# Optimization experiments

Hardware: AMD Instinct MI355X
Metric: run time of the kernel (lower is better)

The kernel has to match this reference:

```python
import jax, jax.numpy as jnp
import numpy as np

SIGMA = 5.0
LOSS_WEIGHT = 1.0


def setup_inputs() -> dict:
    key = jax.random.key(0)
    k1, k2, k3, k4 = jax.random.split(key, 4)
    bs, nj, h, w, d = 4, 22, 64, 64, 64
    return {
        "kpts_gt": jax.random.normal(k1, (bs, 3, nj), dtype=jnp.float32),
        "kpts_pred": jax.random.normal(k2, (bs, 3, nj), dtype=jnp.float32),
        "heatmaps": jax.random.normal(k3, (bs, nj, h, w, d), dtype=jnp.float32),
        "grids": jax.random.normal(k4, (bs, h * w * d, 3), dtype=jnp.float32),
    }


def reference(kpts_gt, kpts_pred, heatmaps, grids):
    bs, nj, h, w, d = heatmaps.shape
    # grids: [bs, h*w*d, 3] -> [bs, 3, h, w, d]
    g = grids.transpose(0, 2, 1).reshape(bs, 3, h, w, d)
    # squared distance via expansion |g - c|^2 = |g|^2 - 2 g.c + |c|^2
    # avoids materializing a [bs, nj, 3, h, w, d] diff tensor
    g2 = jnp.sum(g * g, axis=1)                      # [bs, h, w, d]
    c2 = jnp.sum(kpts_pred * kpts_pred, axis=1)      # [bs, nj]
    gc = jnp.einsum("bchwd,bcj->bjhwd", g, kpts_pred)  # [bs, nj, h, w, d]
    d2 = g2[:, None] - 2.0 * gc + c2[:, :, None, None, None]
    # NOTE: faithful to the original code, the /(2*sigma^2) is applied to the
    # exp result, NOT inside the exponent.
    gaussian_gt = jnp.exp(-d2) / (2.0 * SIGMA ** 2)  # [bs, nj, h, w, d]
    hm = jax.nn.sigmoid(heatmaps)
    loss = 0.5 * jnp.mean((gaussian_gt - hm) ** 2)
    return LOSS_WEIGHT * loss
```

## Files before the change

### kernel.cpp

```cpp
#include <hip/hip_runtime.h>

constexpr int BS  = 4;
constexpr int NJ  = 22;
constexpr int PTS = 64 * 64 * 64;
constexpr int TPB = 256;
constexpr int VEC = 4;
constexpr int BLOCKS_PER_B = PTS / (TPB * VEC);
constexpr int NBLOCKS = BS * BLOCKS_PER_B;
constexpr float INV_2SIG2 = 1.0f / (2.0f * 5.0f * 5.0f);
constexpr long long NELEM = (long long)BS * NJ * PTS;

__global__ __launch_bounds__(TPB) void gauss_loss_main(
    const float* __restrict__ kpts_pred,
    const float* __restrict__ heatmaps,
    const float* __restrict__ grids,
    float* __restrict__ block_sums)
{
    __shared__ float4 cj[NJ];
    const int b   = blockIdx.x / BLOCKS_PER_B;
    const int blk = blockIdx.x % BLOCKS_PER_B;
    const int tid = threadIdx.x;

    if (tid < NJ) {
        const float x = kpts_pred[b * 3 * NJ + 0 * NJ + tid];
        const float y = kpts_pred[b * 3 * NJ + 1 * NJ + tid];
        const float z = kpts_pred[b * 3 * NJ + 2 * NJ + tid];
        cj[tid] = make_float4(x, y, z, x * x + y * y + z * z);
    }
    __syncthreads();

    const int p0 = (blk * TPB + tid) * VEC;

    const float4* gptr = reinterpret_cast<const float4*>(
        grids + (size_t)b * PTS * 3 + (size_t)p0 * 3);
    const float4 ga = gptr[0];
    const float4 gb = gptr[1];
    const float4 gc = gptr[2];

    const float gx[VEC] = {ga.x, ga.w, gb.z, gc.y};
    const float gy[VEC] = {ga.y, gb.x, gb.w, gc.z};
    const float gz[VEC] = {ga.z, gb.y, gc.x, gc.w};
    float g2[VEC];
    #pragma unroll
    for (int i = 0; i < VEC; ++i)
        g2[i] = gx[i] * gx[i] + gy[i] * gy[i] + gz[i] * gz[i];

    const float* hbase = heatmaps + (size_t)b * NJ * PTS + p0;

    float acc = 0.0f;
    #pragma unroll
    for (int j = 0; j < NJ; ++j) {
        const float4 hv = *reinterpret_cast<const float4*>(hbase + (size_t)j * PTS);
        const float h[VEC] = {hv.x, hv.y, hv.z, hv.w};
        const float4 c = cj[j];
        #pragma unroll
        for (int i = 0; i < VEC; ++i) {
            const float dot = gx[i] * c.x + gy[i] * c.y + gz[i] * c.z;
            const float d2  = (g2[i] - 2.0f * dot) + c.w;
            const float gauss = __expf(-d2) * INV_2SIG2;
            const float sg    = __fdividef(1.0f, 1.0f + __expf(-h[i]));
            const float diff  = gauss - sg;
            acc = fmaf(diff, diff, acc);
        }
    }

    #pragma unroll
    for (int off = 32; off > 0; off >>= 1)
        acc += __shfl_down(acc, off, 64);

    __shared__ float wsum[TPB / 64];
    if ((tid & 63) == 0) wsum[tid >> 6] = acc;
    __syncthreads();
    if (tid == 0)
        block_sums[blockIdx.x] = wsum[0] + wsum[1] + wsum[2] + wsum[3];
}

__global__ __launch_bounds__(TPB) void gauss_loss_final(
    const float* __restrict__ block_sums,
    float* __restrict__ out)
{
    const int tid = threadIdx.x;
    float acc = 0.0f;
    for (int i = tid; i < NBLOCKS; i += TPB)
        acc += block_sums[i];

    #pragma unroll
    for (int off = 32; off > 0; off >>= 1)
        acc += __shfl_down(acc, off, 64);

    __shared__ float wsum[TPB / 64];
    if ((tid & 63) == 0) wsum[tid >> 6] = acc;
    __syncthreads();
    if (tid == 0) {
        const float total = wsum[0] + wsum[1] + wsum[2] + wsum[3];
        out[0] = 0.5f * total / (float)NELEM;
    }
}

extern "C" void kernel_launch(void* const* d_in, const int* in_sizes, int n_in,
                              void* d_out, int out_size, void* d_ws, size_t ws_size,
                              hipStream_t stream) {
    const float* kpts_pred = (const float*)d_in[1];
    const float* heatmaps  = (const float*)d_in[2];
    const float* grids     = (const float*)d_in[3];
    float* out = (float*)d_out;
    float* bsums = (float*)d_ws;

    gauss_loss_main<<<NBLOCKS, TPB, 0, stream>>>(kpts_pred, heatmaps, grids, bsums);
    gauss_loss_final<<<1, TPB, 0, stream>>>(bsums, out);
}
```

Before: 150.0 us.

## Split joints across two block halves, fuse final reduction via atomics, prefetch heatmap loads

Doubles the grid by giving each block half of the joints, which gives more waves and more memory parallelism on the 22-way heatmap stream. The separate final reduction kernel is replaced by a memset plus a per-block atomicAdd of the scaled partial sum. The heatmap loads are software-prefetched one joint ahead, and launch bounds request higher occupancy. The cost is that grid points are loaded and recomputed twice, atomic contention grows with 2048 blocks, and the floating-point summation order is no longer deterministic.

Result: slower. 164.6 us (+9.7%).

```diff
diff --git a/kernel.cpp b/kernel.cpp
--- a/kernel.cpp
+++ b/kernel.cpp
@@ -2,24 +2,30 @@
 
 constexpr int BS  = 4;
 constexpr int NJ  = 22;
+constexpr int NJH = 11;
 constexpr int PTS = 64 * 64 * 64;
 constexpr int TPB = 256;
 constexpr int VEC = 4;
 constexpr int BLOCKS_PER_B = PTS / (TPB * VEC);
-constexpr int NBLOCKS = BS * BLOCKS_PER_B;
+constexpr int NBLOCKS_HALF = BS * BLOCKS_PER_B;
+constexpr int NBLOCKS = 2 * NBLOCKS_HALF;
 constexpr float INV_2SIG2 = 1.0f / (2.0f * 5.0f * 5.0f);
 constexpr long long NELEM = (long long)BS * NJ * PTS;
+constexpr float FINAL_SCALE = 0.5f / (float)NELEM;
 
-__global__ __launch_bounds__(TPB) void gauss_loss_main(
+__global__ __launch_bounds__(TPB, 8) void gauss_loss_fused(
     const float* __restrict__ kpts_pred,
     const float* __restrict__ heatmaps,
     const float* __restrict__ grids,
-    float* __restrict__ block_sums)
+    float* __restrict__ out)
 {
     __shared__ float4 cj[NJ];
-    const int b   = blockIdx.x / BLOCKS_PER_B;
-    const int blk = blockIdx.x % BLOCKS_PER_B;
-    const int tid = threadIdx.x;
+    const int bid   = blockIdx.x;
+    const int jh    = bid >> 10;
+    const int inner = bid & 1023;
+    const int b     = inner >> 8;
+    const int blk   = inner & 255;
+    const int tid   = threadIdx.x;
 
     if (tid < NJ) {
         const float x = kpts_pred[b * 3 * NJ + 0 * NJ + tid];
@@ -45,17 +51,23 @@
     for (int i = 0; i < VEC; ++i)
         g2[i] = gx[i] * gx[i] + gy[i] * gy[i] + gz[i] * gz[i];
 
-    const float* hbase = heatmaps + (size_t)b * NJ * PTS + p0;
+    const int j0 = jh * NJH;
+    const float* hbase = heatmaps + (size_t)b * NJ * PTS + (size_t)j0 * PTS + p0;
 
     float acc = 0.0f;
+
+    float4 nxt = *reinterpret_cast<const float4*>(hbase);
     #pragma unroll
-    for (int j = 0; j < NJ; ++j) {
-        const float4 hv = *reinterpret_cast<const float4*>(hbase + (size_t)j * PTS);
-        const float h[VEC] = {hv.x, hv.y, hv.z, hv.w};
-        const float4 c = cj[j];
+    for (int jj = 0; jj < NJH; ++jj) {
+        const float4 cur = nxt;
+        if (jj + 1 < NJH)
+            nxt = *reinterpret_cast<const float4*>(hbase + (size_t)(jj + 1) * PTS);
+
+        const float4 c = cj[j0 + jj];
+        const float h[VEC] = {cur.x, cur.y, cur.z, cur.w};
         #pragma unroll
         for (int i = 0; i < VEC; ++i) {
-            const float dot = gx[i] * c.x + gy[i] * c.y + gz[i] * c.z;
+            const float dot = fmaf(gx[i], c.x, fmaf(gy[i], c.y, gz[i] * c.z));
             const float d2  = (g2[i] - 2.0f * dot) + c.w;
             const float gauss = __expf(-d2) * INV_2SIG2;
             const float sg    = __fdividef(1.0f, 1.0f + __expf(-h[i]));
@@ -71,29 +83,9 @@
     __shared__ float wsum[TPB / 64];
     if ((tid & 63) == 0) wsum[tid >> 6] = acc;
     __syncthreads();
-    if (tid == 0)
-        block_sums[blockIdx.x] = wsum[0] + wsum[1] + wsum[2] + wsum[3];
-}
-
-__global__ __launch_bounds__(TPB) void gauss_loss_final(
-    const float* __restrict__ block_sums,
-    float* __restrict__ out)
-{
-    const int tid = threadIdx.x;
-    float acc = 0.0f;
-    for (int i = tid; i < NBLOCKS; i += TPB)
-        acc += block_sums[i];
-
-    #pragma unroll
-    for (int off = 32; off > 0; off >>= 1)
-        acc += __shfl_down(acc, off, 64);
-
-    __shared__ float wsum[TPB / 64];
-    if ((tid & 63) == 0) wsum[tid >> 6] = acc;
-    __syncthreads();
     if (tid == 0) {
-        const float total = wsum[0] + wsum[1] + wsum[2] + wsum[3];
-        out[0] = 0.5f * total / (float)NELEM;
+        const float partial = wsum[0] + wsum[1] + wsum[2] + wsum[3];
+        atomicAdd(out, partial * FINAL_SCALE);
     }
 }
 
@@ -104,8 +96,7 @@
     const float* heatmaps  = (const float*)d_in[2];
     const float* grids     = (const float*)d_in[3];
     float* out = (float*)d_out;
-    float* bsums = (float*)d_ws;
 
-    gauss_loss_main<<<NBLOCKS, TPB, 0, stream>>>(kpts_pred, heatmaps, grids, bsums);
-    gauss_loss_final<<<1, TPB, 0, stream>>>(bsums, out);
+    hipMemsetAsync(out, 0, sizeof(float), stream);
+    gauss_loss_fused<<<NBLOCKS, TPB, 0, stream>>>(kpts_pred, heatmaps, grids, out);
 }
```

## Replace two-kernel reduction with atomicAdd, add nontemporal loads and FMA dot

Applied to the files above, without the earlier changes.

Drops the second reduction kernel and has each block atomically add its scaled partial sum into the output, which is zeroed first with an async memset. Streaming loads of heatmaps and grids switch to nontemporal builtins, and the dot product is written as explicit FMAs. This removes one kernel launch and the block_sums round trip, but adds a memset operation, 1024 atomics on one address, and a summation order that is no longer deterministic.

After: 150.1 us. About the same (+0.1%).

```diff
diff --git a/kernel.cpp b/kernel.cpp
--- a/kernel.cpp
+++ b/kernel.cpp
@@ -9,12 +9,15 @@
 constexpr int NBLOCKS = BS * BLOCKS_PER_B;
 constexpr float INV_2SIG2 = 1.0f / (2.0f * 5.0f * 5.0f);
 constexpr long long NELEM = (long long)BS * NJ * PTS;
+constexpr float FINAL_SCALE = 0.5f / (float)NELEM;
+
+typedef float f32x4 __attribute__((ext_vector_type(4)));
 
 __global__ __launch_bounds__(TPB) void gauss_loss_main(
     const float* __restrict__ kpts_pred,
     const float* __restrict__ heatmaps,
     const float* __restrict__ grids,
-    float* __restrict__ block_sums)
+    float* __restrict__ out)
 {
     __shared__ float4 cj[NJ];
     const int b   = blockIdx.x / BLOCKS_PER_B;
@@ -31,11 +34,11 @@
 
     const int p0 = (blk * TPB + tid) * VEC;
 
-    const float4* gptr = reinterpret_cast<const float4*>(
+    const f32x4* gptr = reinterpret_cast<const f32x4*>(
         grids + (size_t)b * PTS * 3 + (size_t)p0 * 3);
-    const float4 ga = gptr[0];
-    const float4 gb = gptr[1];
-    const float4 gc = gptr[2];
+    const f32x4 ga = __builtin_nontemporal_load(gptr + 0);
+    const f32x4 gb = __builtin_nontemporal_load(gptr + 1);
+    const f32x4 gc = __builtin_nontemporal_load(gptr + 2);
 
     const float gx[VEC] = {ga.x, ga.w, gb.z, gc.y};
     const float gy[VEC] = {ga.y, gb.x, gb.w, gc.z};
@@ -50,12 +53,13 @@
     float acc = 0.0f;
     #pragma unroll
     for (int j = 0; j < NJ; ++j) {
-        const float4 hv = *reinterpret_cast<const float4*>(hbase + (size_t)j * PTS);
+        const f32x4 hv = __builtin_nontemporal_load(
+            reinterpret_cast<const f32x4*>(hbase + (size_t)j * PTS));
         const float h[VEC] = {hv.x, hv.y, hv.z, hv.w};
         const float4 c = cj[j];
         #pragma unroll
         for (int i = 0; i < VEC; ++i) {
-            const float dot = gx[i] * c.x + gy[i] * c.y + gz[i] * c.z;
+            const float dot = fmaf(gx[i], c.x, fmaf(gy[i], c.y, gz[i] * c.z));
             const float d2  = (g2[i] - 2.0f * dot) + c.w;
             const float gauss = __expf(-d2) * INV_2SIG2;
             const float sg    = __fdividef(1.0f, 1.0f + __expf(-h[i]));
@@ -71,29 +75,9 @@
     __shared__ float wsum[TPB / 64];
     if ((tid & 63) == 0) wsum[tid >> 6] = acc;
     __syncthreads();
-    if (tid == 0)
-        block_sums[blockIdx.x] = wsum[0] + wsum[1] + wsum[2] + wsum[3];
-}
-
-__global__ __launch_bounds__(TPB) void gauss_loss_final(
-    const float* __restrict__ block_sums,
-    float* __restrict__ out)
-{
-    const int tid = threadIdx.x;
-    float acc = 0.0f;
-    for (int i = tid; i < NBLOCKS; i += TPB)
-        acc += block_sums[i];
-
-    #pragma unroll
-    for (int off = 32; off > 0; off >>= 1)
-        acc += __shfl_down(acc, off, 64);
-
-    __shared__ float wsum[TPB / 64];
-    if ((tid & 63) == 0) wsum[tid >> 6] = acc;
-    __syncthreads();
     if (tid == 0) {
-        const float total = wsum[0] + wsum[1] + wsum[2] + wsum[3];
-        out[0] = 0.5f * total / (float)NELEM;
+        const float partial = wsum[0] + wsum[1] + wsum[2] + wsum[3];
+        atomicAdd(out, partial * FINAL_SCALE);
     }
 }
 
@@ -104,8 +88,7 @@
     const float* heatmaps  = (const float*)d_in[2];
     const float* grids     = (const float*)d_in[3];
     float* out = (float*)d_out;
-    float* bsums = (float*)d_ws;
 
-    gauss_loss_main<<<NBLOCKS, TPB, 0, stream>>>(kpts_pred, heatmaps, grids, bsums);
-    gauss_loss_final<<<1, TPB, 0, stream>>>(bsums, out);
+    (void)hipMemsetAsync(out, 0, sizeof(float), stream);
+    gauss_loss_main<<<NBLOCKS, TPB, 0, stream>>>(kpts_pred, heatmaps, grids, out);
 }
```
